# Performance work log

Measured on AMD Instinct MI355X. Metric: run time of the kernel, lower is better.

Reference implementation:

```python
import jax, jax.numpy as jnp
import numpy as np

QLEN, MLEN, BSZ, DMODEL, NHEAD, DHEAD, DFF = 1024, 1024, 4, 1024, 16, 64, 4096
KLEN = QLEN + MLEN


def _layernorm(x, g, b, eps=1e-5):
    mu = jnp.mean(x, axis=-1, keepdims=True)
    var = jnp.var(x, axis=-1, keepdims=True)
    return (x - mu) * jax.lax.rsqrt(var + eps) * g + b


def _rel_shift(x):
    # x: [qlen, klen, bsz, nhead] -- Transformer-XL shift trick
    q, k, b, n = x.shape
    x = jnp.pad(x, ((0, 0), (1, 0), (0, 0), (0, 0)))  # [q, k+1, b, n]
    x = x.reshape(k + 1, q, b, n)[1:]
    return x.reshape(q, k, b, n)


def setup_inputs() -> dict:
    key = jax.random.key(0)
    ks = jax.random.split(key, 16)
    s = 0.02
    inp = {
        "word_embed": jax.random.normal(ks[0], (QLEN, BSZ, DMODEL), jnp.float32),
        "pos_embed": jax.random.normal(ks[1], (KLEN, DMODEL), jnp.float32),
        "bias_q": jax.random.normal(ks[2], (NHEAD, DHEAD), jnp.float32) * s,
        "bias_k": jax.random.normal(ks[3], (NHEAD, DHEAD), jnp.float32) * s,
        "memories": jax.random.normal(ks[4], (MLEN, BSZ, DMODEL), jnp.float32),
        "W_qkv": jax.random.normal(ks[5], (DMODEL, 3 * NHEAD * DHEAD), jnp.float32) * s,
        "W_r": jax.random.normal(ks[6], (DMODEL, NHEAD * DHEAD), jnp.float32) * s,
        "W_o": jax.random.normal(ks[7], (NHEAD * DHEAD, DMODEL), jnp.float32) * s,
        "ln1_g": jnp.ones((DMODEL,), jnp.float32),
        "ln1_b": jnp.zeros((DMODEL,), jnp.float32),
        "W_ff1": jax.random.normal(ks[8], (DMODEL, DFF), jnp.float32) * s,
        "b_ff1": jnp.zeros((DFF,), jnp.float32),
        "W_ff2": jax.random.normal(ks[9], (DFF, DMODEL), jnp.float32) * s,
        "b_ff2": jnp.zeros((DMODEL,), jnp.float32),
        "ln2_g": jnp.ones((DMODEL,), jnp.float32),
        "ln2_b": jnp.zeros((DMODEL,), jnp.float32),
    }
    # causal mask with memory: position i may attend to j <= i + MLEN; True = masked
    i = jnp.arange(QLEN)[:, None]
    j = jnp.arange(KLEN)[None, :]
    inp["attention_mask"] = j > (i + MLEN)
    return inp


def reference(word_embed, pos_embed, bias_q, bias_k, attention_mask, memories,
              W_qkv, W_r, W_o, ln1_g, ln1_b, W_ff1, b_ff1, W_ff2, b_ff2, ln2_g, ln2_b):
    scale = 1.0 / np.sqrt(DHEAD)
    cat = jnp.concatenate([memories, word_embed], axis=0)  # [klen, b, d]
    w_heads = cat @ W_qkv  # [klen, b, 3*n*dh]
    q, k, v = jnp.split(w_heads, 3, axis=-1)
    q = q[-QLEN:].reshape(QLEN, BSZ, NHEAD, DHEAD)
    k = k.reshape(KLEN, BSZ, NHEAD, DHEAD)
    v = v.reshape(KLEN, BSZ, NHEAD, DHEAD)
    r = (pos_embed @ W_r).reshape(KLEN, NHEAD, DHEAD)

    AC = jnp.einsum('ibnd,jbnd->ijbn', q + bias_q, k)          # content term
    BD = jnp.einsum('ibnd,jnd->ijbn', q + bias_k, r)           # position term
    BD = _rel_shift(BD)
    score = (AC + BD) * scale
    score = jnp.where(attention_mask[:, :, None, None], -1e30, score)
    prob = jax.nn.softmax(score, axis=1)
    attn_vec = jnp.einsum('ijbn,jbnd->ibnd', prob, v).reshape(QLEN, BSZ, NHEAD * DHEAD)
    attn_out = attn_vec @ W_o
    out = _layernorm(word_embed + attn_out, ln1_g, ln1_b)       # post-LN (pre_lnorm=False)

    core = jax.nn.relu(out @ W_ff1 + b_ff1) @ W_ff2 + b_ff2
    return _layernorm(out + core, ln2_g, ln2_b)
```

## Files before the change

### kernel.cpp

```cpp
#include <hip/hip_runtime.h>


typedef __bf16 bf16x8 __attribute__((ext_vector_type(8)));
typedef float f32x4 __attribute__((ext_vector_type(4)));

#define DEVI __device__ __forceinline__

DEVI unsigned short f2bf(float f) {
  union { float f; unsigned int u; } v;
  v.f = f;
  unsigned int u = v.u;
  u += 0x7fffu + ((u >> 16) & 1u);
  return (unsigned short)(u >> 16);
}

DEVI void load16(const unsigned short* g, unsigned short* l) {
  __builtin_amdgcn_global_load_lds(
      (const __attribute__((address_space(1))) unsigned int*)g,
      (__attribute__((address_space(3))) unsigned int*)l, 16, 0, 0);
}

__global__ __launch_bounds__(256) void cvt_bf16_kernel(const float* __restrict__ in,
                                                       unsigned short* __restrict__ out) {
  const int i = blockIdx.x * 256 + threadIdx.x;
  float4 v = *(const float4*)(in + (size_t)i * 4);
  ushort4 o;
  o.x = f2bf(v.x);
  o.y = f2bf(v.y);
  o.z = f2bf(v.z);
  o.w = f2bf(v.w);
  *(ushort4*)(out + (size_t)i * 4) = o;
}

template <typename T>
__global__ __launch_bounds__(256) void transpose_to_bf16(
    const T* __restrict__ in, unsigned short* __restrict__ out, int R, int C) {
  __shared__ unsigned short t[64][72];
  const int tid = threadIdx.x;
  const size_t zoff = (size_t)blockIdx.z * R * C;
  const int r0 = blockIdx.y * 64, c0 = blockIdx.x * 64;
  const T* inp = in + zoff;
  unsigned short* outp = out + zoff;
#pragma unroll
  for (int it = 0; it < 4; ++it) {
    int f = tid + 256 * it;
    int r = f >> 4;
    int c4 = (f & 15) << 2;
    if constexpr (sizeof(T) == 4) {
      float4 v = *(const float4*)((const float*)inp + (size_t)(r0 + r) * C + c0 + c4);
      t[c4 + 0][r] = f2bf(v.x);
      t[c4 + 1][r] = f2bf(v.y);
      t[c4 + 2][r] = f2bf(v.z);
      t[c4 + 3][r] = f2bf(v.w);
    } else {
      ushort4 v = *(const ushort4*)((const unsigned short*)inp + (size_t)(r0 + r) * C + c0 + c4);
      t[c4 + 0][r] = v.x;
      t[c4 + 1][r] = v.y;
      t[c4 + 2][r] = v.z;
      t[c4 + 3][r] = v.w;
    }
  }
  __syncthreads();
#pragma unroll
  for (int it = 0; it < 4; ++it) {
    int f = tid + 256 * it;
    int cc = f >> 4;
    int r4 = (f & 15) << 2;
    ushort4 o;
    o.x = t[cc][r4 + 0];
    o.y = t[cc][r4 + 1];
    o.z = t[cc][r4 + 2];
    o.w = t[cc][r4 + 3];
    *(ushort4*)(outp + (size_t)(c0 + cc) * R + r0 + r4) = o;
  }
}

struct GemmArgs {
  const unsigned short* A;
  const unsigned short* Bt;
  int row_split;
  int M, N, K;
  const float* p0;
  const float* p1;
  const float* resid;
  float* outF;
  unsigned short* o0;
  unsigned short* o1;
  unsigned short* o2;
  unsigned short* o3;
  int relu;
};

constexpr int BM = 128, BN = 128, BK = 64;

template <int EPI>
__global__ __launch_bounds__(256, 4) void gemm_kernel(GemmArgs ga) {
  __shared__ __align__(16) unsigned short As[BM * BK];
  __shared__ __align__(16) unsigned short Bs[BN * BK];

  const int n0 = blockIdx.x * BN;
  const int m0 = blockIdx.y * BM;
  if constexpr (EPI == 0) {
    if (n0 + BN <= 1024 && m0 + BM <= ga.row_split) return;
  }
  const int tid = threadIdx.x;
  const int lane = tid & 63;
  const int wv = tid >> 6;
  const int l15 = lane & 15;
  const int quad = lane >> 4;
  const int wm = wv & 1, wn = wv >> 1;
  const int K = ga.K;
  const int r8 = lane >> 3;
  const int sc = (lane & 7) ^ r8;

  const f32x4 fzero = {0.f, 0.f, 0.f, 0.f};
  f32x4 acc[4][4];
#pragma unroll
  for (int i = 0; i < 4; ++i)
#pragma unroll
    for (int j = 0; j < 4; ++j) acc[i][j] = fzero;

  const unsigned short* Ab = ga.A + (size_t)(m0 + 32 * wv + r8) * K + sc * 8;
  const unsigned short* Bb = ga.Bt + (size_t)(n0 + 32 * wv + r8) * K + sc * 8;
  const int h7 = l15 & 7;

  for (int k0 = 0; k0 < K; k0 += BK) {
    __syncthreads();
#pragma unroll
    for (int it = 0; it < 4; ++it)
      load16(Ab + (size_t)(8 * it) * K + k0, &As[(32 * wv + 8 * it) * 64]);
#pragma unroll
    for (int it = 0; it < 4; ++it)
      load16(Bb + (size_t)(8 * it) * K + k0, &Bs[(32 * wv + 8 * it) * 64]);
    __syncthreads();
#pragma unroll
    for (int ks = 0; ks < 2; ++ks) {
      bf16x8 af[4], bg[4];
#pragma unroll
      for (int mt = 0; mt < 4; ++mt)
        af[mt] = *(const bf16x8*)&As[(wm * 64 + mt * 16 + l15) * 64 +
                                     (((ks * 4 + quad) ^ h7) * 8)];
#pragma unroll
      for (int nt = 0; nt < 4; ++nt)
        bg[nt] = *(const bf16x8*)&Bs[(wn * 64 + nt * 16 + l15) * 64 +
                                     (((ks * 4 + quad) ^ h7) * 8)];
#pragma unroll
      for (int mt = 0; mt < 4; ++mt)
#pragma unroll
        for (int nt = 0; nt < 4; ++nt)
          acc[mt][nt] =
              __builtin_amdgcn_mfma_f32_16x16x32_bf16(af[mt], bg[nt], acc[mt][nt], 0, 0, 0);
    }
  }

#pragma unroll
  for (int mt = 0; mt < 4; ++mt) {
#pragma unroll
    for (int nt = 0; nt < 4; ++nt) {
#pragma unroll
      for (int r = 0; r < 4; ++r) {
        const int row = m0 + wm * 64 + mt * 16 + quad * 4 + r;
        const int col = n0 + wn * 64 + nt * 16 + l15;
        float val = acc[mt][nt][r];
        if constexpr (EPI == 0) {
          const int seq = row >> 2, b = row & 3;
          if (col < 1024) {
            if (seq >= 1024) {
              const int nh = col >> 6, d = col & 63;
              const size_t o = ((size_t)((b * 16 + nh) * 1024 + (seq - 1024))) * 64 + d;
              ga.o0[o] = f2bf(val + ga.p0[col]);
              ga.o1[o] = f2bf(val + ga.p1[col]);
            }
          } else if (col < 2048) {
            const int c = col - 1024, nh = c >> 6, d = c & 63, bn = b * 16 + nh;
            const size_t o = (size_t)bn * 131072 +
                             (size_t)(((seq >> 4) * 2 + (d >> 5)) * 512) +
                             ((((d >> 3) & 3) * 16 + (seq & 15)) * 8) + (d & 7);
            ga.o2[o] = f2bf(val);
          } else {
            const int c = col - 2048, nh = c >> 6, d = c & 63, bn = b * 16 + nh;
            const size_t o = (size_t)bn * 131072 + (size_t)((seq >> 7) * 8192) +
                             ((((seq >> 5) & 3) * 4 + (d >> 4)) * 512) +
                             ((((seq >> 3) & 3) * 16 + (d & 15)) * 8) + (seq & 7);
            ga.o3[o] = f2bf(val);
          }
        } else if constexpr (EPI == 1) {
          const int nh = col >> 6, d = col & 63, t = row;
          const size_t o = (size_t)nh * 131072 +
                           (size_t)(((t >> 4) * 2 + (d >> 5)) * 512) +
                           ((((d >> 3) & 3) * 16 + (t & 15)) * 8) + (d & 7);
          ga.o0[o] = f2bf(val);
        } else {
          if (ga.p0) val += ga.p0[col];
          if (ga.resid) val += ga.resid[(size_t)row * ga.N + col];
          if (ga.relu) val = fmaxf(val, 0.f);
          if (ga.outF) ga.outF[(size_t)row * ga.N + col] = val;
          if (ga.o0) ga.o0[(size_t)row * ga.N + col] = f2bf(val);
        }
      }
    }
  }
}

constexpr int P_LD = 136;
constexpr float CEXP = 0.18033688f;

__global__ __launch_bounds__(256, 4) void attn_kernel(
    const unsigned short* __restrict__ QQ, const unsigned short* __restrict__ QK,
    const unsigned short* __restrict__ Kf, const unsigned short* __restrict__ Vf,
    const unsigned short* __restrict__ Rf, unsigned short* __restrict__ AVb) {
  __shared__ __align__(16) unsigned short p_s[4][16 * P_LD];

  const int tid = threadIdx.x;
  const int lane = tid & 63;
  const int wv = tid >> 6;
  const int l15 = lane & 15;
  const int quad = lane >> 4;
  const int bn = blockIdx.x;
  const int iw = (blockIdx.y * 4 + wv) * 16;
  const int nh = bn & 15;
  const int bb = bn >> 4;
  unsigned short* pw = &p_s[wv][0];

  const unsigned short* kf = Kf + (size_t)bn * 131072;
  const unsigned short* vf = Vf + (size_t)bn * 131072;
  const unsigned short* rf = Rf + (size_t)nh * 131072;

  const size_t qoff = (size_t)bn * (1024 * 64) + (size_t)(iw + l15) * 64;
  const bf16x8 qq0 = *(const bf16x8*)(QQ + qoff + quad * 8);
  const bf16x8 qq1 = *(const bf16x8*)(QQ + qoff + 32 + quad * 8);
  const bf16x8 qk0 = *(const bf16x8*)(QK + qoff + quad * 8);
  const bf16x8 qk1 = *(const bf16x8*)(QK + qoff + 32 + quad * 8);

  const f32x4 fzero = {0.f, 0.f, 0.f, 0.f};
  f32x4 o_acc[4];
#pragma unroll
  for (int i = 0; i < 4; ++i) o_acc[i] = fzero;
  float lsum[4] = {0.f, 0.f, 0.f, 0.f};

  const int lane8 = lane * 8;
  const int jmax = iw + 15 + 1024;
  for (int j0 = 0; j0 <= jmax; j0 += 128) {
    const int t16b = (j0 >> 4) + 63 - (iw >> 4);
    f32x4 bd[9];
#pragma unroll
    for (int ct = 0; ct < 9; ++ct) {
      int tg = t16b + ct;
      tg = (tg < 127) ? tg : 127;
      const unsigned short* rb = rf + (size_t)(tg * 1024) + lane8;
      bf16x8 b0 = *(const bf16x8*)rb;
      bf16x8 b1 = *(const bf16x8*)(rb + 512);
      f32x4 c = fzero;
      c = __builtin_amdgcn_mfma_f32_16x16x32_bf16(qk0, b0, c, 0, 0, 0);
      c = __builtin_amdgcn_mfma_f32_16x16x32_bf16(qk1, b1, c, 0, 0, 0);
      bd[ct] = c;
    }

    const int ntb = j0 >> 4;
    f32x4 sv[8];
#pragma unroll
    for (int nt = 0; nt < 8; ++nt) {
      const unsigned short* kb = kf + (size_t)((ntb + nt) * 1024) + lane8;
      bf16x8 b0 = *(const bf16x8*)kb;
      bf16x8 b1 = *(const bf16x8*)(kb + 512);
      f32x4 c = fzero;
      c = __builtin_amdgcn_mfma_f32_16x16x32_bf16(qq0, b0, c, 0, 0, 0);
      c = __builtin_amdgcn_mfma_f32_16x16x32_bf16(qq1, b1, c, 0, 0, 0);
      sv[nt] = c;
    }

#pragma unroll
    for (int r = 0; r < 4; ++r) {
      const int il = quad * 4 + r;
      const int u = l15 + 15 - il;
      const int srcl = (lane & 48) | (u & 15);
      float w[9];
#pragma unroll
      for (int ct = 0; ct < 9; ++ct) w[ct] = __shfl(bd[ct][r], srcl, 64);
      const int ig = iw + il;
#pragma unroll
      for (int nt = 0; nt < 8; ++nt) {
        const float bdv = (u & 16) ? w[nt + 1] : w[nt];
        const int jg = j0 + nt * 16 + l15;
        float p = exp2f((sv[nt][r] + bdv) * CEXP);
        p = (jg > ig + 1024) ? 0.f : p;
        lsum[r] += p;
        pw[il * P_LD + nt * 16 + l15] = f2bf(p);
      }
    }

    const unsigned short* vb = vf + (size_t)((j0 >> 7) * 8192) + lane8;
#pragma unroll
    for (int ks = 0; ks < 4; ++ks) {
      bf16x8 ap = *(const bf16x8*)&pw[l15 * P_LD + ks * 32 + quad * 8];
#pragma unroll
      for (int nto = 0; nto < 4; ++nto) {
        bf16x8 bv = *(const bf16x8*)(vb + (ks * 4 + nto) * 512);
        o_acc[nto] = __builtin_amdgcn_mfma_f32_16x16x32_bf16(ap, bv, o_acc[nto], 0, 0, 0);
      }
    }
  }

  float linv[4];
#pragma unroll
  for (int r = 0; r < 4; ++r) {
    float l = lsum[r];
    l += __shfl_xor(l, 1, 64);
    l += __shfl_xor(l, 2, 64);
    l += __shfl_xor(l, 4, 64);
    l += __shfl_xor(l, 8, 64);
    linv[r] = 1.f / l;
  }
#pragma unroll
  for (int nto = 0; nto < 4; ++nto) {
#pragma unroll
    for (int r = 0; r < 4; ++r) {
      const int ig = iw + quad * 4 + r;
      const int d = nto * 16 + l15;
      const float val = o_acc[nto][r] * linv[r];
      AVb[(size_t)(ig * 4 + bb) * 1024 + nh * 64 + d] = f2bf(val);
    }
  }
}

__global__ __launch_bounds__(256) void ln_kernel(const float* __restrict__ x,
                                                 const float* __restrict__ g,
                                                 const float* __restrict__ bta,
                                                 float* __restrict__ outF,
                                                 unsigned short* __restrict__ outB) {
  const int row = blockIdx.x;
  const int tid = threadIdx.x;
  const float* xr = x + (size_t)row * 1024;
  const float4 v = *(const float4*)(xr + tid * 4);
  float s = v.x + v.y + v.z + v.w;
  float ss = v.x * v.x + v.y * v.y + v.z * v.z + v.w * v.w;
#pragma unroll
  for (int off = 1; off < 64; off <<= 1) {
    s += __shfl_xor(s, off, 64);
    ss += __shfl_xor(ss, off, 64);
  }
  __shared__ float red[8];
  const int wv = tid >> 6;
  if ((tid & 63) == 0) {
    red[wv] = s;
    red[4 + wv] = ss;
  }
  __syncthreads();
  s = red[0] + red[1] + red[2] + red[3];
  ss = red[4] + red[5] + red[6] + red[7];
  const float mu = s * (1.f / 1024.f);
  const float var = ss * (1.f / 1024.f) - mu * mu;
  const float rs = rsqrtf(var + 1e-5f);
  const float vv[4] = {v.x, v.y, v.z, v.w};
#pragma unroll
  for (int u = 0; u < 4; ++u) {
    const int c = tid * 4 + u;
    const float y = (vv[u] - mu) * rs * g[c] + bta[c];
    if (outF) outF[(size_t)row * 1024 + c] = y;
    if (outB) outB[(size_t)row * 1024 + c] = f2bf(y);
  }
}

extern "C" void kernel_launch(void* const* d_in, const int* in_sizes, int n_in,
                              void* d_out, int out_size, void* d_ws, size_t ws_size,
                              hipStream_t stream) {
  (void)in_sizes; (void)n_in; (void)out_size; (void)ws_size;
  const float* word_embed = (const float*)d_in[0];
  const float* pos_embed = (const float*)d_in[1];
  const float* bias_q = (const float*)d_in[2];
  const float* bias_k = (const float*)d_in[3];
  const float* memories = (const float*)d_in[4];
  const float* W_qkv = (const float*)d_in[5];
  const float* W_r = (const float*)d_in[6];
  const float* W_o = (const float*)d_in[7];
  const float* ln1_g = (const float*)d_in[8];
  const float* ln1_b = (const float*)d_in[9];
  const float* W_ff1 = (const float*)d_in[10];
  const float* b_ff1 = (const float*)d_in[11];
  const float* W_ff2 = (const float*)d_in[12];
  const float* b_ff2 = (const float*)d_in[13];
  const float* ln2_g = (const float*)d_in[14];
  const float* ln2_b = (const float*)d_in[15];
  float* out = (float*)d_out;

  char* ws = (char*)d_ws;
  unsigned short* QQ = (unsigned short*)(ws + 0);
  unsigned short* QK = (unsigned short*)(ws + 8388608);
  unsigned short* Kf = (unsigned short*)(ws + 16777216);
  unsigned short* Vf = (unsigned short*)(ws + 50331648);
  unsigned short* Rf = (unsigned short*)(ws + 67108864);
  unsigned short* AVb = (unsigned short*)(ws + 71303168);
  float* X1 = (float*)(ws + 79691776);
  float* OUT1 = (float*)(ws + 96468992);
  unsigned short* OUT1b = (unsigned short*)(ws + 113246208);
  unsigned short* Wqkv_t = (unsigned short*)(ws + 121634816);
  unsigned short* Wr_t = (unsigned short*)(ws + 127926272);
  unsigned short* Wo_t = (unsigned short*)(ws + 130023424);
  unsigned short* Wff1_t = (unsigned short*)(ws + 132120576);
  unsigned short* Wff2_t = (unsigned short*)(ws + 140509184);
  unsigned short* Catb = (unsigned short*)(ws + 79691776);
  unsigned short* Posb = (unsigned short*)(ws + 96468992);
  unsigned short* H = (unsigned short*)(ws + 0);
  float* C2 = X1;

  const dim3 blk(256);

  cvt_bf16_kernel<<<4096, blk, 0, stream>>>(memories, Catb);
  cvt_bf16_kernel<<<4096, blk, 0, stream>>>(word_embed, Catb + (size_t)4096 * 1024);
  cvt_bf16_kernel<<<2048, blk, 0, stream>>>(pos_embed, Posb);

  transpose_to_bf16<float><<<dim3(48, 16, 1), blk, 0, stream>>>(W_qkv, Wqkv_t, 1024, 3072);
  transpose_to_bf16<float><<<dim3(16, 16, 1), blk, 0, stream>>>(W_r, Wr_t, 1024, 1024);
  transpose_to_bf16<float><<<dim3(16, 16, 1), blk, 0, stream>>>(W_o, Wo_t, 1024, 1024);
  transpose_to_bf16<float><<<dim3(64, 16, 1), blk, 0, stream>>>(W_ff1, Wff1_t, 1024, 4096);
  transpose_to_bf16<float><<<dim3(16, 64, 1), blk, 0, stream>>>(W_ff2, Wff2_t, 4096, 1024);

  {
    GemmArgs a{};
    a.A = Catb;
    a.row_split = 4096;
    a.Bt = Wqkv_t;
    a.M = 8192; a.N = 3072; a.K = 1024;
    a.p0 = bias_q; a.p1 = bias_k;
    a.o0 = QQ; a.o1 = QK; a.o2 = Kf; a.o3 = Vf;
    gemm_kernel<0><<<dim3(24, 64), blk, 0, stream>>>(a);
  }
  {
    GemmArgs a{};
    a.A = Posb;
    a.Bt = Wr_t;
    a.M = 2048; a.N = 1024; a.K = 1024;
    a.o0 = Rf;
    gemm_kernel<1><<<dim3(8, 16), blk, 0, stream>>>(a);
  }

  attn_kernel<<<dim3(64, 16), blk, 0, stream>>>(QQ, QK, Kf, Vf, Rf, AVb);

  {
    GemmArgs a{};
    a.A = AVb;
    a.Bt = Wo_t;
    a.M = 4096; a.N = 1024; a.K = 1024;
    a.resid = word_embed;
    a.outF = X1;
    gemm_kernel<2><<<dim3(8, 32), blk, 0, stream>>>(a);
  }
  ln_kernel<<<4096, blk, 0, stream>>>(X1, ln1_g, ln1_b, OUT1, OUT1b);

  {
    GemmArgs a{};
    a.A = OUT1b;
    a.Bt = Wff1_t;
    a.M = 4096; a.N = 4096; a.K = 1024;
    a.p0 = b_ff1;
    a.relu = 1;
    a.o0 = H;
    gemm_kernel<2><<<dim3(32, 32), blk, 0, stream>>>(a);
  }
  {
    GemmArgs a{};
    a.A = H;
    a.Bt = Wff2_t;
    a.M = 4096; a.N = 1024; a.K = 4096;
    a.p0 = b_ff2;
    a.resid = OUT1;
    a.outF = C2;
    gemm_kernel<2><<<dim3(8, 32), blk, 0, stream>>>(a);
  }
  ln_kernel<<<4096, blk, 0, stream>>>(C2, ln2_g, ln2_b, out, nullptr);
}
```

Measured before the change: 684.9 us.

## Split attention key range across waves with split-K reduction in shared memory

Each block now handles 32 query rows, and its four waves take interleaved 128-wide key chunks instead of separate query rows. Partial outputs and row sums are combined through shared memory at the end. The grid grows to 32 blocks in y, launched in reverse order so the long causal rows start first. The aim is better load balance and sharing of K/V/R reads across the block, at the cost of an extra reduction, two syncthreads, and more registers for the two query halves.

```diff
diff --git a/kernel.cpp b/kernel.cpp
--- a/kernel.cpp
+++ b/kernel.cpp
@@ -209,7 +209,7 @@
     const unsigned short* __restrict__ QQ, const unsigned short* __restrict__ QK,
     const unsigned short* __restrict__ Kf, const unsigned short* __restrict__ Vf,
     const unsigned short* __restrict__ Rf, unsigned short* __restrict__ AVb) {
-  __shared__ __align__(16) unsigned short p_s[4][16 * P_LD];
+  __shared__ __align__(16) unsigned short smem[4 * 32 * P_LD];
 
   const int tid = threadIdx.x;
   const int lane = tid & 63;
@@ -217,109 +217,195 @@
   const int l15 = lane & 15;
   const int quad = lane >> 4;
   const int bn = blockIdx.x;
-  const int iw = (blockIdx.y * 4 + wv) * 16;
+  const int ib = (31 - blockIdx.y) * 32;
   const int nh = bn & 15;
   const int bb = bn >> 4;
-  unsigned short* pw = &p_s[wv][0];
+  unsigned short* pw = smem + wv * 32 * P_LD;
 
   const unsigned short* kf = Kf + (size_t)bn * 131072;
   const unsigned short* vf = Vf + (size_t)bn * 131072;
   const unsigned short* rf = Rf + (size_t)nh * 131072;
 
-  const size_t qoff = (size_t)bn * (1024 * 64) + (size_t)(iw + l15) * 64;
-  const bf16x8 qq0 = *(const bf16x8*)(QQ + qoff + quad * 8);
-  const bf16x8 qq1 = *(const bf16x8*)(QQ + qoff + 32 + quad * 8);
-  const bf16x8 qk0 = *(const bf16x8*)(QK + qoff + quad * 8);
-  const bf16x8 qk1 = *(const bf16x8*)(QK + qoff + 32 + quad * 8);
+  bf16x8 qq[2][2], qk[2][2];
+#pragma unroll
+  for (int h = 0; h < 2; ++h) {
+    const size_t qoff = (size_t)bn * (1024 * 64) + (size_t)(ib + 16 * h + l15) * 64;
+    qq[h][0] = *(const bf16x8*)(QQ + qoff + quad * 8);
+    qq[h][1] = *(const bf16x8*)(QQ + qoff + 32 + quad * 8);
+    qk[h][0] = *(const bf16x8*)(QK + qoff + quad * 8);
+    qk[h][1] = *(const bf16x8*)(QK + qoff + 32 + quad * 8);
+  }
 
   const f32x4 fzero = {0.f, 0.f, 0.f, 0.f};
-  f32x4 o_acc[4];
-#pragma unroll
-  for (int i = 0; i < 4; ++i) o_acc[i] = fzero;
-  float lsum[4] = {0.f, 0.f, 0.f, 0.f};
+  f32x4 o_acc[2][4];
+#pragma unroll
+  for (int h = 0; h < 2; ++h)
+#pragma unroll
+    for (int i = 0; i < 4; ++i) o_acc[h][i] = fzero;
+  float lsum[2][4] = {{0.f, 0.f, 0.f, 0.f}, {0.f, 0.f, 0.f, 0.f}};
 
   const int lane8 = lane * 8;
-  const int jmax = iw + 15 + 1024;
-  for (int j0 = 0; j0 <= jmax; j0 += 128) {
-    const int t16b = (j0 >> 4) + 63 - (iw >> 4);
-    f32x4 bd[9];
-#pragma unroll
-    for (int ct = 0; ct < 9; ++ct) {
-      int tg = t16b + ct;
-      tg = (tg < 127) ? tg : 127;
-      const unsigned short* rb = rf + (size_t)(tg * 1024) + lane8;
-      bf16x8 b0 = *(const bf16x8*)rb;
-      bf16x8 b1 = *(const bf16x8*)(rb + 512);
-      f32x4 c = fzero;
-      c = __builtin_amdgcn_mfma_f32_16x16x32_bf16(qk0, b0, c, 0, 0, 0);
-      c = __builtin_amdgcn_mfma_f32_16x16x32_bf16(qk1, b1, c, 0, 0, 0);
-      bd[ct] = c;
-    }
-
+  const int jmax = ib + 31 + 1024;
+  for (int j0 = wv * 128; j0 <= jmax; j0 += 512) {
     const int ntb = j0 >> 4;
-    f32x4 sv[8];
-#pragma unroll
-    for (int nt = 0; nt < 8; ++nt) {
-      const unsigned short* kb = kf + (size_t)((ntb + nt) * 1024) + lane8;
-      bf16x8 b0 = *(const bf16x8*)kb;
-      bf16x8 b1 = *(const bf16x8*)(kb + 512);
-      f32x4 c = fzero;
-      c = __builtin_amdgcn_mfma_f32_16x16x32_bf16(qq0, b0, c, 0, 0, 0);
-      c = __builtin_amdgcn_mfma_f32_16x16x32_bf16(qq1, b1, c, 0, 0, 0);
-      sv[nt] = c;
-    }
-
-#pragma unroll
-    for (int r = 0; r < 4; ++r) {
-      const int il = quad * 4 + r;
-      const int u = l15 + 15 - il;
-      const int srcl = (lane & 48) | (u & 15);
-      float w[9];
-#pragma unroll
-      for (int ct = 0; ct < 9; ++ct) w[ct] = __shfl(bd[ct][r], srcl, 64);
-      const int ig = iw + il;
-#pragma unroll
-      for (int nt = 0; nt < 8; ++nt) {
-        const float bdv = (u & 16) ? w[nt + 1] : w[nt];
-        const int jg = j0 + nt * 16 + l15;
-        float p = exp2f((sv[nt][r] + bdv) * CEXP);
-        p = (jg > ig + 1024) ? 0.f : p;
-        lsum[r] += p;
-        pw[il * P_LD + nt * 16 + l15] = f2bf(p);
+#pragma unroll
+    for (int h = 0; h < 2; ++h) {
+      const int ih = ib + 16 * h;
+      const int t16b = ntb + 63 - (ih >> 4);
+      f32x4 bd[5];
+#pragma unroll
+      for (int ct = 0; ct < 5; ++ct) {
+        int tg = t16b + ct;
+        tg = (tg < 127) ? tg : 127;
+        const unsigned short* rb = rf + (size_t)(tg * 1024) + lane8;
+        bf16x8 b0 = *(const bf16x8*)rb;
+        bf16x8 b1 = *(const bf16x8*)(rb + 512);
+        f32x4 c = fzero;
+        c = __builtin_amdgcn_mfma_f32_16x16x32_bf16(qk[h][0], b0, c, 0, 0, 0);
+        c = __builtin_amdgcn_mfma_f32_16x16x32_bf16(qk[h][1], b1, c, 0, 0, 0);
+        bd[ct] = c;
+      }
+      f32x4 sv[4];
+#pragma unroll
+      for (int nt = 0; nt < 4; ++nt) {
+        const unsigned short* kb = kf + (size_t)((ntb + nt) * 1024) + lane8;
+        bf16x8 b0 = *(const bf16x8*)kb;
+        bf16x8 b1 = *(const bf16x8*)(kb + 512);
+        f32x4 c = fzero;
+        c = __builtin_amdgcn_mfma_f32_16x16x32_bf16(qq[h][0], b0, c, 0, 0, 0);
+        c = __builtin_amdgcn_mfma_f32_16x16x32_bf16(qq[h][1], b1, c, 0, 0, 0);
+        sv[nt] = c;
+      }
+#pragma unroll
+      for (int r = 0; r < 4; ++r) {
+        const int il = quad * 4 + r;
+        const int u = l15 + 15 - il;
+        const int srcl = (lane & 48) | (u & 15);
+        float w[5];
+#pragma unroll
+        for (int ct = 0; ct < 5; ++ct) w[ct] = __shfl(bd[ct][r], srcl, 64);
+        const int ig = ih + il;
+#pragma unroll
+        for (int nt = 0; nt < 4; ++nt) {
+          const float bdv = (u & 16) ? w[nt + 1] : w[nt];
+          const int jg = j0 + nt * 16 + l15;
+          float p = exp2f((sv[nt][r] + bdv) * CEXP);
+          p = (jg > ig + 1024) ? 0.f : p;
+          lsum[h][r] += p;
+          pw[(h * 16 + il) * P_LD + nt * 16 + l15] = f2bf(p);
+        }
+      }
+      f32x4 bdB[5];
+      bdB[0] = bd[4];
+#pragma unroll
+      for (int ct = 1; ct < 5; ++ct) {
+        int tg = t16b + 4 + ct;
+        tg = (tg < 127) ? tg : 127;
+        const unsigned short* rb = rf + (size_t)(tg * 1024) + lane8;
+        bf16x8 b0 = *(const bf16x8*)rb;
+        bf16x8 b1 = *(const bf16x8*)(rb + 512);
+        f32x4 c = fzero;
+        c = __builtin_amdgcn_mfma_f32_16x16x32_bf16(qk[h][0], b0, c, 0, 0, 0);
+        c = __builtin_amdgcn_mfma_f32_16x16x32_bf16(qk[h][1], b1, c, 0, 0, 0);
+        bdB[ct] = c;
+      }
+#pragma unroll
+      for (int nt = 0; nt < 4; ++nt) {
+        const unsigned short* kb = kf + (size_t)((ntb + nt + 4) * 1024) + lane8;
+        bf16x8 b0 = *(const bf16x8*)kb;
+        bf16x8 b1 = *(const bf16x8*)(kb + 512);
+        f32x4 c = fzero;
+        c = __builtin_amdgcn_mfma_f32_16x16x32_bf16(qq[h][0], b0, c, 0, 0, 0);
+        c = __builtin_amdgcn_mfma_f32_16x16x32_bf16(qq[h][1], b1, c, 0, 0, 0);
+        sv[nt] = c;
+      }
+#pragma unroll
+      for (int r = 0; r < 4; ++r) {
+        const int il = quad * 4 + r;
+        const int u = l15 + 15 - il;
+        const int srcl = (lane & 48) | (u & 15);
+        float w[5];
+#pragma unroll
+        for (int ct = 0; ct < 5; ++ct) w[ct] = __shfl(bdB[ct][r], srcl, 64);
+        const int ig = ih + il;
+#pragma unroll
+        for (int nt = 0; nt < 4; ++nt) {
+          const float bdv = (u & 16) ? w[nt + 1] : w[nt];
+          const int jg = j0 + (nt + 4) * 16 + l15;
+          float p = exp2f((sv[nt][r] + bdv) * CEXP);
+          p = (jg > ig + 1024) ? 0.f : p;
+          lsum[h][r] += p;
+          pw[(h * 16 + il) * P_LD + (nt + 4) * 16 + l15] = f2bf(p);
+        }
       }
     }
 
     const unsigned short* vb = vf + (size_t)((j0 >> 7) * 8192) + lane8;
 #pragma unroll
     for (int ks = 0; ks < 4; ++ks) {
-      bf16x8 ap = *(const bf16x8*)&pw[l15 * P_LD + ks * 32 + quad * 8];
+      bf16x8 ap0 = *(const bf16x8*)&pw[l15 * P_LD + ks * 32 + quad * 8];
+      bf16x8 ap1 = *(const bf16x8*)&pw[(16 + l15) * P_LD + ks * 32 + quad * 8];
 #pragma unroll
       for (int nto = 0; nto < 4; ++nto) {
         bf16x8 bv = *(const bf16x8*)(vb + (ks * 4 + nto) * 512);
-        o_acc[nto] = __builtin_amdgcn_mfma_f32_16x16x32_bf16(ap, bv, o_acc[nto], 0, 0, 0);
-      }
-    }
-  }
-
-  float linv[4];
-#pragma unroll
-  for (int r = 0; r < 4; ++r) {
-    float l = lsum[r];
-    l += __shfl_xor(l, 1, 64);
-    l += __shfl_xor(l, 2, 64);
-    l += __shfl_xor(l, 4, 64);
-    l += __shfl_xor(l, 8, 64);
-    linv[r] = 1.f / l;
-  }
-#pragma unroll
-  for (int nto = 0; nto < 4; ++nto) {
+        o_acc[0][nto] = __builtin_amdgcn_mfma_f32_16x16x32_bf16(ap0, bv, o_acc[0][nto], 0, 0, 0);
+        o_acc[1][nto] = __builtin_amdgcn_mfma_f32_16x16x32_bf16(ap1, bv, o_acc[1][nto], 0, 0, 0);
+      }
+    }
+  }
+
+  float lred[2][4];
+#pragma unroll
+  for (int h = 0; h < 2; ++h) {
 #pragma unroll
     for (int r = 0; r < 4; ++r) {
-      const int ig = iw + quad * 4 + r;
-      const int d = nto * 16 + l15;
-      const float val = o_acc[nto][r] * linv[r];
-      AVb[(size_t)(ig * 4 + bb) * 1024 + nh * 64 + d] = f2bf(val);
-    }
+      float l = lsum[h][r];
+      l += __shfl_xor(l, 1, 64);
+      l += __shfl_xor(l, 2, 64);
+      l += __shfl_xor(l, 4, 64);
+      l += __shfl_xor(l, 8, 64);
+      lred[h][r] = l;
+    }
+  }
+
+  __syncthreads();
+  float* Ops = (float*)smem;
+  float* Lp = ((float*)smem) + 4 * 64 * 33;
+  {
+    float* op = Ops + (size_t)(wv * 64 + lane) * 33;
+#pragma unroll
+    for (int h = 0; h < 2; ++h)
+#pragma unroll
+      for (int nto = 0; nto < 4; ++nto)
+#pragma unroll
+        for (int r = 0; r < 4; ++r) op[h * 16 + nto * 4 + r] = o_acc[h][nto][r];
+    if (l15 == 0) {
+#pragma unroll
+      for (int h = 0; h < 2; ++h)
+#pragma unroll
+        for (int r = 0; r < 4; ++r) Lp[wv * 32 + h * 16 + quad * 4 + r] = lred[h][r];
+    }
+  }
+  __syncthreads();
+
+  {
+    const int il = tid >> 3;
+    const int d0 = (tid & 7) * 8;
+    const int h = il >> 4, r = il & 3, q2 = (il >> 2) & 3;
+    const float L = Lp[il] + Lp[32 + il] + Lp[64 + il] + Lp[96 + il];
+    const float linv = 1.f / L;
+    unsigned short obuf[8];
+#pragma unroll
+    for (int dd = 0; dd < 8; ++dd) {
+      const int d = d0 + dd;
+      const int srcl = q2 * 16 + (d & 15);
+      const int idx = h * 16 + (d >> 4) * 4 + r;
+      float s = Ops[(size_t)srcl * 33 + idx] + Ops[(size_t)(64 + srcl) * 33 + idx] +
+                Ops[(size_t)(128 + srcl) * 33 + idx] + Ops[(size_t)(192 + srcl) * 33 + idx];
+      obuf[dd] = f2bf(s * linv);
+    }
+    const int ig = ib + il;
+    *(uint4*)&AVb[(size_t)(ig * 4 + bb) * 1024 + nh * 64 + d0] = *(const uint4*)obuf;
   }
 }
 
@@ -434,7 +520,7 @@
     gemm_kernel<1><<<dim3(8, 16), blk, 0, stream>>>(a);
   }
 
-  attn_kernel<<<dim3(64, 16), blk, 0, stream>>>(QQ, QK, Kf, Vf, Rf, AVb);
+  attn_kernel<<<dim3(64, 32), blk, 0, stream>>>(QQ, QK, Kf, Vf, Rf, AVb);
 
   {
     GemmArgs a{};
```

Result: slower. 780.3 us (+13.9%).
